# Kernel optimization log

Measured on AMD Instinct MI355X. Metric: run time of the kernel, lower is better.

Reference implementation:

```python
import jax, jax.numpy as jnp
import numpy as np

VOCAB, EMBED, HIDDEN = 32000, 512, 1024
B, T = 32, 512


def setup_inputs() -> dict:
    key = jax.random.key(0)
    k1, k2, k3, k4, k5, k6 = jax.random.split(key, 6)
    s_ih = 1.0 / np.sqrt(HIDDEN)
    return {
        "input_ids": jax.random.randint(k1, (B, T), 0, VOCAB, dtype=jnp.int32),
        "h0": jax.random.normal(k2, (1, B, HIDDEN), dtype=jnp.float32),
        "c0": jax.random.normal(k3, (1, B, HIDDEN), dtype=jnp.float32),
        "emb": jax.random.normal(k4, (VOCAB, EMBED), dtype=jnp.float32),
        # PyTorch LSTM weights: weight_ih [4H, E], weight_hh [4H, H], gate order i,f,g,o; bias=False
        "W_ih": jax.random.uniform(k5, (4 * HIDDEN, EMBED), dtype=jnp.float32, minval=-s_ih, maxval=s_ih),
        "W_hh": jax.random.uniform(k6, (4 * HIDDEN, HIDDEN), dtype=jnp.float32, minval=-s_ih, maxval=s_ih),
    }


def _lstm(x, h0, c0, W_ih, W_hh):
    # x: [B,T,E]; precompute input projections once (the only big GEMM)
    x_proj = jnp.einsum("bte,ge->tbg", x, W_ih)  # [T,B,4H]
    H = W_hh.shape[1]

    def step(carry, xt):
        h, c = carry
        gates = xt + h @ W_hh.T  # [B,4H]
        i, f, g, o = jnp.split(gates, 4, axis=-1)
        c = jax.nn.sigmoid(f) * c + jax.nn.sigmoid(i) * jnp.tanh(g)
        h = jax.nn.sigmoid(o) * jnp.tanh(c)
        return (h, c), h

    (hn, cn), ys = jax.lax.scan(step, (h0, c0), x_proj)
    return jnp.transpose(ys, (1, 0, 2)), hn, cn  # output [B,T,H]


def reference(input_ids, h0, c0, emb, W_ih, W_hh):
    embedded = emb[input_ids]  # [B,T,E] embedding lookup
    output, hn, cn = _lstm(embedded, h0[0], c0[0], W_ih, W_hh)
    return output, hn[None], cn[None]
```

## Files before the change

### kernel.cpp

```cpp
#include <hip/hip_runtime.h>
#include <hip/hip_bf16.h>
#include <hip/hip_cooperative_groups.h>

#define E   512
#define H   1024
#define BB  32
#define TT  512
#define G4  4096
#define YS_ELEMS 16777216

typedef __attribute__((ext_vector_type(8))) short bf16x8;
typedef __attribute__((ext_vector_type(4))) float f32x4;

__device__ __forceinline__ unsigned short f2bf(float x){
    union { float f; unsigned u; } v; v.f = x;
    unsigned r = v.u + 0x7fffu + ((v.u >> 16) & 1u);
    return (unsigned short)(r >> 16);
}
__device__ __forceinline__ float bf2f(unsigned short b){
    union { unsigned u; float f; } v; v.u = ((unsigned)b) << 16;
    return v.f;
}
__device__ __forceinline__ float sigm(float x){ return 1.f/(1.f+__expf(-x)); }
__device__ __forceinline__ float tanh_(float x){ return 2.f/(1.f+__expf(-2.f*x)) - 1.f; }

__global__ void k_prep(const int* __restrict__ ids, const float* __restrict__ emb,
                       const float* __restrict__ Wih, const float* __restrict__ Whh,
                       const float* __restrict__ h0,
                       unsigned short* __restrict__ Abf, unsigned short* __restrict__ Bbf,
                       unsigned short* __restrict__ Wb,  unsigned short* __restrict__ hb,
                       unsigned* __restrict__ flags)
{
    int bx = blockIdx.x, tx = threadIdx.x;
    if (bx == 0) flags[tx] = 0;
    const float* src; unsigned short* dst;
    if (bx < 4096) {
        unsigned u = bx*256u + tx;
        int m  = u >> 6;
        int e0 = (u & 63) * 8;
        int row = ids[(m & 31) * TT + (m >> 5)];
        src = emb + (size_t)row * E + e0;
        dst = Abf + (size_t)m   * E + e0;
    } else if (bx < 5120) {
        size_t off = ((size_t)(bx-4096)*256u + tx) * 8;
        src = Wih + off; dst = Bbf + off;
    } else if (bx < 7168) {
        size_t off = ((size_t)(bx-5120)*256u + tx) * 8;
        src = Whh + off; dst = Wb + off;
    } else {
        size_t off = ((size_t)(bx-7168)*256u + tx) * 8;
        src = h0 + off; dst = hb + off;
    }
    float4 f0 = *(const float4*)(src);
    float4 f1 = *(const float4*)(src + 4);
    uint4 o;
    o.x = f2bf(f0.x) | ((unsigned)f2bf(f0.y) << 16);
    o.y = f2bf(f0.z) | ((unsigned)f2bf(f0.w) << 16);
    o.z = f2bf(f1.x) | ((unsigned)f2bf(f1.y) << 16);
    o.w = f2bf(f1.z) | ((unsigned)f2bf(f1.w) << 16);
    *(uint4*)dst = o;
}

__global__ __launch_bounds__(256) void k_gemm(const unsigned short* __restrict__ A,
        const unsigned short* __restrict__ Bm, unsigned short* __restrict__ C)
{
    __shared__ __align__(16) unsigned short As[128][40];
    __shared__ __align__(16) unsigned short Bs[128][40];
    int tid = threadIdx.x;
    int bm = blockIdx.x & 127;
    int bn = blockIdx.x >> 7;
    int w = tid >> 6, lane = tid & 63, l15 = lane & 15, quad = lane >> 4;
    int wm = w & 1, wn = w >> 1;
    f32x4 acc[4][4] = {};
    for (int kt = 0; kt < 16; ++kt) {
        __syncthreads();
        for (int i = 0; i < 2; ++i) {
            int c = tid + 256*i;
            int row = c >> 2, kc = (c & 3) * 8;
            *(uint4*)&As[row][kc] = *(const uint4*)(A  + ((size_t)(bm*128 + row))*E + kt*32 + kc);
            *(uint4*)&Bs[row][kc] = *(const uint4*)(Bm + ((size_t)(bn*128 + row))*E + kt*32 + kc);
        }
        __syncthreads();
        bf16x8 af[4], bfr[4];
        for (int i = 0; i < 4; ++i) af[i]  = *(const bf16x8*)&As[wm*64 + i*16 + l15][quad*8];
        for (int j = 0; j < 4; ++j) bfr[j] = *(const bf16x8*)&Bs[wn*64 + j*16 + l15][quad*8];
        for (int i = 0; i < 4; ++i)
            for (int j = 0; j < 4; ++j)
                acc[i][j] = __builtin_amdgcn_mfma_f32_16x16x32_bf16(af[i], bfr[j], acc[i][j], 0,0,0);
    }
    for (int i = 0; i < 4; ++i)
        for (int j = 0; j < 4; ++j)
            for (int r = 0; r < 4; ++r) {
                int mg = bm*128 + wm*64 + i*16 + quad*4 + r;
                int ng = bn*128 + wn*64 + j*16 + l15;
                C[(size_t)mg * G4 + ng] = f2bf(acc[i][j][r]);
            }
}

__global__ __launch_bounds__(256, 1) void k_recur(const unsigned short* __restrict__ xp,
        const unsigned short* __restrict__ Wb, unsigned short* __restrict__ hbuf,
        const float* __restrict__ c0, float* __restrict__ out,
        unsigned* __restrict__ flags)
{
    __shared__ __align__(16) unsigned short Ws[16][1032];
    __shared__ float gbuf[2][32][17];
    int tid = threadIdx.x;
    int blk = blockIdx.x;
    int w = tid >> 6, lane = tid & 63, l15 = lane & 15, quad = lane >> 4;
    int kh = w >> 1, m0 = (w & 1) * 16;

    for (int c = 0; c < 8; ++c) {
        int id = tid + 256*c;
        int n = id >> 7, kc = (id & 127) * 8;
        int grow = (n >> 2) * H + blk*4 + (n & 3);
        *(uint4*)&Ws[n][kc] = *(const uint4*)(Wb + (size_t)grow * H + kc);
    }
    int b  = tid & 31;
    int kp = (tid >> 5) & 1;
    int kg0 = blk*4 + kp*2;
    float cA = 0.f, cB = 0.f;
    if (tid < 64) {
        float2 cc = *(const float2*)(c0 + b*H + kg0);
        cA = cc.x; cB = cc.y;
    }
    __syncthreads();

    for (int t = 0; t < TT; ++t) {
        const unsigned short* cur = hbuf + (t & 1) * (BB*H);
        unsigned short*       nxt = hbuf + ((t+1) & 1) * (BB*H);
        float xA[4], xB[4];
        if (tid < 64) {
            #pragma unroll
            for (int q = 0; q < 4; ++q) {
                unsigned x2 = *(const unsigned*)(xp + ((size_t)t*BB + b)*G4 + q*H + kg0);
                xA[q] = bf2f((unsigned short)(x2 & 0xffffu));
                xB[q] = bf2f((unsigned short)(x2 >> 16));
            }
        }
        if (tid < 64) {
            unsigned tgt = (unsigned)t;
            const unsigned* fp = flags + lane*4;
            bool ok;
            do {
                unsigned f0 = __hip_atomic_load(fp+0, __ATOMIC_RELAXED, __HIP_MEMORY_SCOPE_AGENT);
                unsigned f1 = __hip_atomic_load(fp+1, __ATOMIC_RELAXED, __HIP_MEMORY_SCOPE_AGENT);
                unsigned f2 = __hip_atomic_load(fp+2, __ATOMIC_RELAXED, __HIP_MEMORY_SCOPE_AGENT);
                unsigned f3 = __hip_atomic_load(fp+3, __ATOMIC_RELAXED, __HIP_MEMORY_SCOPE_AGENT);
                ok = (f0 >= tgt) & (f1 >= tgt) & (f2 >= tgt) & (f3 >= tgt);
            } while (!__all(ok));
        }
        __syncthreads();
        f32x4 acc = {};
        {
            const unsigned short* pa = cur + (size_t)(m0 + l15)*H + kh*512 + quad*8;
            bf16x8 av[16];
#define LDA(i, o) asm volatile("global_load_dwordx4 %0, %1, off offset:" o " sc0 sc1" \
                               : "=v"(av[i]) : "v"(pa))
            LDA(0,"0");    LDA(1,"64");   LDA(2,"128");  LDA(3,"192");
            LDA(4,"256");  LDA(5,"320");  LDA(6,"384");  LDA(7,"448");
            LDA(8,"512");  LDA(9,"576");  LDA(10,"640"); LDA(11,"704");
            LDA(12,"768"); LDA(13,"832"); LDA(14,"896"); LDA(15,"960");
#undef LDA
            bf16x8 bv[16];
            #pragma unroll
            for (int k2 = 0; k2 < 16; ++k2)
                bv[k2] = *(const bf16x8*)&Ws[l15][(kh*16 + k2)*32 + quad*8];
            asm volatile("s_waitcnt vmcnt(0)" ::: "memory");
            __builtin_amdgcn_sched_barrier(0);
            #pragma unroll
            for (int k2 = 0; k2 < 16; ++k2)
                acc = __builtin_amdgcn_mfma_f32_16x16x32_bf16(av[k2], bv[k2], acc, 0,0,0);
        }
        #pragma unroll
        for (int r = 0; r < 4; ++r)
            gbuf[kh][m0 + quad*4 + r][l15] = acc[r];
        __syncthreads();
        if (tid < 64) {
            float pA[4], pB[4];
            #pragma unroll
            for (int q = 0; q < 4; ++q) {
                int ca = q*4 + kp*2;
                pA[q] = gbuf[0][b][ca]   + gbuf[1][b][ca]   + xA[q];
                pB[q] = gbuf[0][b][ca+1] + gbuf[1][b][ca+1] + xB[q];
            }
            float iA = sigm(pA[0]), fA = sigm(pA[1]), gA = tanh_(pA[2]), oA = sigm(pA[3]);
            float iB = sigm(pB[0]), fB = sigm(pB[1]), gB = tanh_(pB[2]), oB = sigm(pB[3]);
            cA = fA * cA + iA * gA;
            cB = fB * cB + iB * gB;
            float hA = oA * tanh_(cA);
            float hB = oB * tanh_(cB);
            unsigned hp = (unsigned)f2bf(hA) | ((unsigned)f2bf(hB) << 16);
            __hip_atomic_store((unsigned*)(nxt + b*H + kg0), hp,
                               __ATOMIC_RELAXED, __HIP_MEMORY_SCOPE_AGENT);
            asm volatile("s_waitcnt vmcnt(0)" ::: "memory");
            if (tid == 0)
                __hip_atomic_store(&flags[blk], (unsigned)(t+1),
                                   __ATOMIC_RELAXED, __HIP_MEMORY_SCOPE_AGENT);
            *(float2*)(out + (size_t)b*(TT*H) + (size_t)t*H + kg0) = make_float2(hA, hB);
            if (t == TT-1) {
                *(float2*)(out + YS_ELEMS + b*H + kg0)         = make_float2(hA, hB);
                *(float2*)(out + YS_ELEMS + 32768 + b*H + kg0) = make_float2(cA, cB);
            }
        }
    }
}

extern "C" void kernel_launch(void* const* d_in, const int* in_sizes, int n_in,
                              void* d_out, int out_size, void* d_ws, size_t ws_size,
                              hipStream_t stream)
{
    const int*   ids = (const int*)  d_in[0];
    const float* h0  = (const float*)d_in[1];
    const float* c0  = (const float*)d_in[2];
    const float* emb = (const float*)d_in[3];
    const float* Wih = (const float*)d_in[4];
    const float* Whh = (const float*)d_in[5];
    float* out = (float*)d_out;
    char* ws = (char*)d_ws;
    unsigned short* xp  = (unsigned short*)(ws);
    unsigned short* Abf = (unsigned short*)(ws + 134217728);
    unsigned short* Bbf = (unsigned short*)(ws + 134217728 + 16777216);
    unsigned short* Wb  = (unsigned short*)(ws + 134217728 + 16777216 + 4194304);
    unsigned short* hb  = (unsigned short*)(ws + 134217728 + 16777216 + 4194304 + 8388608);
    unsigned*       fl  = (unsigned*)      (ws + 134217728 + 16777216 + 4194304 + 8388608 + 131072);

    k_prep<<<7184, 256, 0, stream>>>(ids, emb, Wih, Whh, h0, Abf, Bbf, Wb, hb, fl);
    k_gemm<<<4096, 256, 0, stream>>>(Abf, Bbf, xp);
    void* args[] = { (void*)&xp, (void*)&Wb, (void*)&hb, (void*)&c0, (void*)&out, (void*)&fl };
    hipLaunchCooperativeKernel((void*)k_recur, dim3(256), dim3(256), args, 0, stream);
}
```

Baseline: 2.761 ms.

## Keep recurrent weights in registers and relayout input projections per block

The recurrent kernel now loads its W_hh slice straight into VGPRs once, instead of staging it in LDS and re-reading LDS every timestep. The GEMM epilogue writes x_proj in a block-major layout, so each recurrent block's per-step input values sit in one contiguous 1 KB chunk loaded with raw asm. The flag poll becomes a single vector load that bypasses the cache. Together these aim to cut per-step latency on the serial critical path, at the cost of more register pressure and tying the x_proj layout to the block mapping.

```diff
diff --git a/kernel.cpp b/kernel.cpp
--- a/kernel.cpp
+++ b/kernel.cpp
@@ -93,7 +93,10 @@
             for (int r = 0; r < 4; ++r) {
                 int mg = bm*128 + wm*64 + i*16 + quad*4 + r;
                 int ng = bn*128 + wn*64 + j*16 + l15;
-                C[(size_t)mg * G4 + ng] = f2bf(acc[i][j][r]);
+                int t2 = mg >> 5, b2 = mg & 31;
+                int q  = ng >> 10, col = ng & 1023;
+                C[((size_t)(t2*256 + (col>>2)))*512 + q*128 + b2*4 + (col&3)]
+                    = f2bf(acc[i][j][r]);
             }
 }
 
@@ -102,18 +105,25 @@
         const float* __restrict__ c0, float* __restrict__ out,
         unsigned* __restrict__ flags)
 {
-    __shared__ __align__(16) unsigned short Ws[16][1032];
     __shared__ float gbuf[2][32][17];
     int tid = threadIdx.x;
     int blk = blockIdx.x;
     int w = tid >> 6, lane = tid & 63, l15 = lane & 15, quad = lane >> 4;
     int kh = w >> 1, m0 = (w & 1) * 16;
 
-    for (int c = 0; c < 8; ++c) {
-        int id = tid + 256*c;
-        int n = id >> 7, kc = (id & 127) * 8;
-        int grow = (n >> 2) * H + blk*4 + (n & 3);
-        *(uint4*)&Ws[n][kc] = *(const uint4*)(Wb + (size_t)grow * H + kc);
+    bf16x8 wf[16];
+    {
+        const unsigned short* wp = Wb
+            + (size_t)((l15 >> 2)*H + blk*4 + (l15 & 3))*H + kh*512 + quad*8;
+#define WLD(i, O) asm volatile("global_load_dwordx4 %0, %1, off offset:" O \
+                               : "=v"(wf[i]) : "v"(wp))
+        WLD(0,"0");    WLD(1,"64");   WLD(2,"128");  WLD(3,"192");
+        WLD(4,"256");  WLD(5,"320");  WLD(6,"384");  WLD(7,"448");
+        WLD(8,"512");  WLD(9,"576");  WLD(10,"640"); WLD(11,"704");
+        WLD(12,"768"); WLD(13,"832"); WLD(14,"896"); WLD(15,"960");
+#undef WLD
+        asm volatile("s_waitcnt vmcnt(0)" ::: "memory");
+        __builtin_amdgcn_sched_barrier(0);
     }
     int b  = tid & 31;
     int kp = (tid >> 5) & 1;
@@ -128,26 +138,25 @@
     for (int t = 0; t < TT; ++t) {
         const unsigned short* cur = hbuf + (t & 1) * (BB*H);
         unsigned short*       nxt = hbuf + ((t+1) & 1) * (BB*H);
-        float xA[4], xB[4];
+        unsigned xw0, xw1, xw2, xw3;
         if (tid < 64) {
-            #pragma unroll
-            for (int q = 0; q < 4; ++q) {
-                unsigned x2 = *(const unsigned*)(xp + ((size_t)t*BB + b)*G4 + q*H + kg0);
-                xA[q] = bf2f((unsigned short)(x2 & 0xffffu));
-                xB[q] = bf2f((unsigned short)(x2 >> 16));
-            }
+            const char* xb = (const char*)xp + ((size_t)t*256 + blk)*1024 + b*8 + kp*4;
+            asm volatile("global_load_dword %0, %1, off"            : "=v"(xw0) : "v"(xb));
+            asm volatile("global_load_dword %0, %1, off offset:256" : "=v"(xw1) : "v"(xb));
+            asm volatile("global_load_dword %0, %1, off offset:512" : "=v"(xw2) : "v"(xb));
+            asm volatile("global_load_dword %0, %1, off offset:768" : "=v"(xw3) : "v"(xb));
         }
         if (tid < 64) {
             unsigned tgt = (unsigned)t;
-            const unsigned* fp = flags + lane*4;
-            bool ok;
-            do {
-                unsigned f0 = __hip_atomic_load(fp+0, __ATOMIC_RELAXED, __HIP_MEMORY_SCOPE_AGENT);
-                unsigned f1 = __hip_atomic_load(fp+1, __ATOMIC_RELAXED, __HIP_MEMORY_SCOPE_AGENT);
-                unsigned f2 = __hip_atomic_load(fp+2, __ATOMIC_RELAXED, __HIP_MEMORY_SCOPE_AGENT);
-                unsigned f3 = __hip_atomic_load(fp+3, __ATOMIC_RELAXED, __HIP_MEMORY_SCOPE_AGENT);
-                ok = (f0 >= tgt) & (f1 >= tgt) & (f2 >= tgt) & (f3 >= tgt);
-            } while (!__all(ok));
+            const char* fp = (const char*)(flags + lane*4);
+            uint4 f;
+            for (;;) {
+                asm volatile("global_load_dwordx4 %0, %1, off sc0 sc1"
+                             : "=v"(f) : "v"(fp));
+                asm volatile("s_waitcnt vmcnt(0)" ::: "memory");
+                bool ok = (f.x >= tgt) & (f.y >= tgt) & (f.z >= tgt) & (f.w >= tgt);
+                if (__all(ok)) break;
+            }
         }
         __syncthreads();
         f32x4 acc = {};
@@ -161,21 +170,22 @@
             LDA(8,"512");  LDA(9,"576");  LDA(10,"640"); LDA(11,"704");
             LDA(12,"768"); LDA(13,"832"); LDA(14,"896"); LDA(15,"960");
 #undef LDA
-            bf16x8 bv[16];
-            #pragma unroll
-            for (int k2 = 0; k2 < 16; ++k2)
-                bv[k2] = *(const bf16x8*)&Ws[l15][(kh*16 + k2)*32 + quad*8];
             asm volatile("s_waitcnt vmcnt(0)" ::: "memory");
             __builtin_amdgcn_sched_barrier(0);
             #pragma unroll
             for (int k2 = 0; k2 < 16; ++k2)
-                acc = __builtin_amdgcn_mfma_f32_16x16x32_bf16(av[k2], bv[k2], acc, 0,0,0);
+                acc = __builtin_amdgcn_mfma_f32_16x16x32_bf16(av[k2], wf[k2], acc, 0,0,0);
         }
         #pragma unroll
         for (int r = 0; r < 4; ++r)
             gbuf[kh][m0 + quad*4 + r][l15] = acc[r];
         __syncthreads();
         if (tid < 64) {
+            float xA[4], xB[4];
+            xA[0] = bf2f((unsigned short)(xw0 & 0xffffu)); xB[0] = bf2f((unsigned short)(xw0 >> 16));
+            xA[1] = bf2f((unsigned short)(xw1 & 0xffffu)); xB[1] = bf2f((unsigned short)(xw1 >> 16));
+            xA[2] = bf2f((unsigned short)(xw2 & 0xffffu)); xB[2] = bf2f((unsigned short)(xw2 >> 16));
+            xA[3] = bf2f((unsigned short)(xw3 & 0xffffu)); xB[3] = bf2f((unsigned short)(xw3 >> 16));
             float pA[4], pB[4];
             #pragma unroll
             for (int q = 0; q < 4; ++q) {
```

New measurement: 3.216 ms. +16.5%, slower.
